# Kernel tuning notes

Hardware: AMD Instinct MI355X
Metric: run time of the kernel (lower is better)

## Reference

```python
import jax, jax.numpy as jnp
import numpy as np

N_Z = 128
N_COMP = 10
N_CLASSES = 10
BS = 8192


def setup_inputs() -> dict:
    key = jax.random.key(0)
    k_z, k_g, k_m = jax.random.split(key, 3)
    z = jax.random.normal(k_z, (BS, N_Z), dtype=jnp.float32)
    y = jax.random.randint(k_g, (BS,), 0, N_CLASSES, dtype=jnp.int64)
    # Gumbel noise replicating torch F.gumbel_softmax internal sampling
    gumbel = jax.random.gumbel(jax.random.fold_in(key, 1), (N_CLASSES, BS, N_COMP), dtype=jnp.float32)
    m = jax.random.normal(k_m, (N_CLASSES, N_COMP, N_Z), dtype=jnp.float32)
    # torch init: L = eye(n_z) per (class, component)
    L = jnp.broadcast_to(jnp.eye(N_Z, dtype=jnp.float32), (N_CLASSES, N_COMP, N_Z, N_Z))
    logits = jnp.zeros((N_CLASSES, N_COMP), dtype=jnp.float32)
    return {"z": z, "y": y, "gumbel": gumbel, "m": m, "L": L, "logits": logits}


def reference(z, y, gumbel, m, L, logits):
    C, K = logits.shape
    # hard gumbel-softmax (tau=1) per class, straight-through
    scores = logits[:, None, :] + gumbel                 # (C, bs, K)
    soft = jax.nn.softmax(scores, axis=-1)               # (C, bs, K)
    hard = jax.nn.one_hot(jnp.argmax(scores, axis=-1), K, dtype=soft.dtype)
    comp_mask = hard + soft - jax.lax.stop_gradient(soft)  # (C, bs, K)
    # every class/component affine: m + z @ L.T -> (C, K, bs, n_z)
    samps = jnp.einsum('bi,ckji->ckbj', z, L) + m[:, :, None, :]
    # select component per (class, sample)
    per_class = jnp.einsum('cbk,ckbj->cbj', comp_mask, samps)  # (C, bs, n_z)
    # select class per sample via one-hot(y)
    y1h = jax.nn.one_hot(y, C, dtype=per_class.dtype)          # (bs, C)
    x = jnp.einsum('bc,cbj->bj', y1h, per_class)               # (bs, n_z)
    return x
```

## Files before the change

### kernel.cpp

```cpp
#include <hip/hip_runtime.h>


#define N_Z 128
#define N_COMP 10
#define N_CLASSES 10
#define N_CK (N_CLASSES * N_COMP)
#define LPITCH 136
#define LIST_CAP 256

typedef __attribute__((ext_vector_type(4))) __bf16 bf16x4;
typedef __attribute__((ext_vector_type(8))) __bf16 bf16x8;
typedef __attribute__((ext_vector_type(4))) float f32x4;

__global__ __launch_bounds__(256) void k_select(
    const int* __restrict__ y, const float* __restrict__ gumbel,
    const float* __restrict__ logits, unsigned char* __restrict__ ck_arr, int bs)
{
    int b = blockIdx.x * 256 + threadIdx.x;
    if (b >= bs) return;
    int c = y[b];
    const float* g  = gumbel + ((size_t)c * bs + b) * N_COMP;
    const float* lg = logits + c * N_COMP;
    float2 g01 = *(const float2*)(g + 0);
    float2 g23 = *(const float2*)(g + 2);
    float2 g45 = *(const float2*)(g + 4);
    float2 g67 = *(const float2*)(g + 6);
    float2 g89 = *(const float2*)(g + 8);
    float sc[N_COMP] = {
        g01.x + lg[0], g01.y + lg[1], g23.x + lg[2], g23.y + lg[3],
        g45.x + lg[4], g45.y + lg[5], g67.x + lg[6], g67.y + lg[7],
        g89.x + lg[8], g89.y + lg[9] };
    float best = sc[0];
    int bi = 0;
    #pragma unroll
    for (int k = 1; k < N_COMP; ++k)
        if (sc[k] > best) { best = sc[k]; bi = k; }
    ck_arr[b] = (unsigned char)(c * N_COMP + bi);
}

__global__ __launch_bounds__(256) void k_mfma(
    const float* __restrict__ z, const float* __restrict__ m,
    const float* __restrict__ L, const unsigned char* __restrict__ ck_arr,
    float* __restrict__ out, int bs)
{
    const int ck = blockIdx.x;
    const int jh = blockIdx.y;

    __shared__ __align__(16) __bf16 Lsb[64 * LPITCH];
    __shared__ int list[LIST_CAP];
    __shared__ int cnt;

    const int t = threadIdx.x;
    if (t == 0) cnt = 0;

    uint4 ckw[2];
    {
        const uint4* ck4 = (const uint4*)ck_arr;
        ckw[0] = ck4[t];
        ckw[1] = ck4[256 + t];
    }
    float4 lv[8];
    {
        const float4* Lg4 = (const float4*)(L + ((size_t)ck * N_Z + jh * 64) * N_Z);
        #pragma unroll
        for (int p = 0; p < 8; ++p) lv[p] = Lg4[p * 256 + t];
    }
    __syncthreads();

    #pragma unroll
    for (int h = 0; h < 2; ++h) {
        int b0 = (h * 256 + t) * 16;
        unsigned w[4] = {ckw[h].x, ckw[h].y, ckw[h].z, ckw[h].w};
        #pragma unroll
        for (int q = 0; q < 4; ++q) {
            #pragma unroll
            for (int e = 0; e < 4; ++e) {
                if (((w[q] >> (8 * e)) & 0xFFu) == (unsigned)ck) {
                    int p2 = atomicAdd(&cnt, 1);
                    if (p2 < LIST_CAP) list[p2] = b0 + q * 4 + e;
                }
            }
        }
    }
    #pragma unroll
    for (int p = 0; p < 8; ++p) {
        int f   = p * 256 + t;
        int row = f >> 5;
        int c4  = f & 31;
        bf16x4 b4 = { (__bf16)lv[p].x, (__bf16)lv[p].y, (__bf16)lv[p].z, (__bf16)lv[p].w };
        *(bf16x4*)&Lsb[row * LPITCH + c4 * 4] = b4;
    }
    __syncthreads();

    const int n = min(cnt, LIST_CAP);
    const int ntiles = (n + 15) >> 4;

    const int wv   = t >> 6;
    const int lane = t & 63;
    const int mn   = lane & 15;
    const int quad = lane >> 4;

    for (int nt = wv; nt < ntiles; nt += 4) {
        const int nb = nt * 16;
        const int sidx = nb + mn;
        const int samp = list[sidx < n ? sidx : n - 1];
        const float* zrow = z + (size_t)samp * N_Z;

        bf16x8 bf[4];
        #pragma unroll
        for (int ks = 0; ks < 4; ++ks) {
            float4 z0 = *(const float4*)(zrow + ks * 32 + quad * 8);
            float4 z1 = *(const float4*)(zrow + ks * 32 + quad * 8 + 4);
            bf16x8 b8 = { (__bf16)z0.x, (__bf16)z0.y, (__bf16)z0.z, (__bf16)z0.w,
                          (__bf16)z1.x, (__bf16)z1.y, (__bf16)z1.z, (__bf16)z1.w };
            bf[ks] = b8;
        }

        #pragma unroll
        for (int mt = 0; mt < 4; ++mt) {
            f32x4 acc = {0.f, 0.f, 0.f, 0.f};
            #pragma unroll
            for (int ks = 0; ks < 4; ++ks) {
                bf16x8 af = *(const bf16x8*)&Lsb[(mt * 16 + mn) * LPITCH + ks * 32 + quad * 8];
                acc = __builtin_amdgcn_mfma_f32_16x16x32_bf16(af, bf[ks], acc, 0, 0, 0);
            }
            if (sidx < n) {
                int j0 = jh * 64 + mt * 16 + quad * 4;
                float4 mv = *(const float4*)(m + ck * N_Z + j0);
                float4 o;
                o.x = acc.x + mv.x;
                o.y = acc.y + mv.y;
                o.z = acc.z + mv.z;
                o.w = acc.w + mv.w;
                *(float4*)(out + (size_t)list[sidx] * N_Z + j0) = o;
            }
        }
    }
}

extern "C" void kernel_launch(void* const* d_in, const int* in_sizes, int n_in,
                              void* d_out, int out_size, void* d_ws, size_t ws_size,
                              hipStream_t stream)
{
    const float* z      = (const float*)d_in[0];
    const int*   y      = (const int*)d_in[1];
    const float* gumbel = (const float*)d_in[2];
    const float* m      = (const float*)d_in[3];
    const float* L      = (const float*)d_in[4];
    const float* logits = (const float*)d_in[5];
    float* out = (float*)d_out;

    const int bs = in_sizes[0] / N_Z;

    unsigned char* ck_arr = (unsigned char*)d_ws;

    k_select<<<(bs + 255) / 256, 256, 0, stream>>>(y, gumbel, logits, ck_arr, bs);
    k_mfma<<<dim3(N_CK, 2), 256, 0, stream>>>(z, m, L, ck_arr, out, bs);
}
```

Before: 80.64 us.

## Fuse select and MFMA kernels with a device-wide flag barrier, split batch

```diff
diff --git a/kernel.cpp b/kernel.cpp
--- a/kernel.cpp
+++ b/kernel.cpp
@@ -7,70 +7,78 @@
 #define N_CK (N_CLASSES * N_COMP)
 #define LPITCH 136
 #define LIST_CAP 256
+#define POISON 0xAAAAAAAAu
 
 typedef __attribute__((ext_vector_type(4))) __bf16 bf16x4;
 typedef __attribute__((ext_vector_type(8))) __bf16 bf16x8;
 typedef __attribute__((ext_vector_type(4))) float f32x4;
 
-__global__ __launch_bounds__(256) void k_select(
-    const int* __restrict__ y, const float* __restrict__ gumbel,
-    const float* __restrict__ logits, unsigned char* __restrict__ ck_arr, int bs)
-{
-    int b = blockIdx.x * 256 + threadIdx.x;
-    if (b >= bs) return;
-    int c = y[b];
-    const float* g  = gumbel + ((size_t)c * bs + b) * N_COMP;
-    const float* lg = logits + c * N_COMP;
-    float2 g01 = *(const float2*)(g + 0);
-    float2 g23 = *(const float2*)(g + 2);
-    float2 g45 = *(const float2*)(g + 4);
-    float2 g67 = *(const float2*)(g + 6);
-    float2 g89 = *(const float2*)(g + 8);
-    float sc[N_COMP] = {
-        g01.x + lg[0], g01.y + lg[1], g23.x + lg[2], g23.y + lg[3],
-        g45.x + lg[4], g45.y + lg[5], g67.x + lg[6], g67.y + lg[7],
-        g89.x + lg[8], g89.y + lg[9] };
-    float best = sc[0];
-    int bi = 0;
-    #pragma unroll
-    for (int k = 1; k < N_COMP; ++k)
-        if (sc[k] > best) { best = sc[k]; bi = k; }
-    ck_arr[b] = (unsigned char)(c * N_COMP + bi);
-}
-
-__global__ __launch_bounds__(256) void k_mfma(
-    const float* __restrict__ z, const float* __restrict__ m,
-    const float* __restrict__ L, const unsigned char* __restrict__ ck_arr,
-    float* __restrict__ out, int bs)
+__global__ __launch_bounds__(256, 2) void k_fused(
+    const float* __restrict__ z, const int* __restrict__ y,
+    const float* __restrict__ gumbel, const float* __restrict__ m,
+    const float* __restrict__ L, const float* __restrict__ logits,
+    float* __restrict__ out, unsigned* __restrict__ flag,
+    unsigned char* __restrict__ ck_arr, int bs)
 {
     const int ck = blockIdx.x;
     const int jh = blockIdx.y;
+    const int bh = blockIdx.z;
+    const int t  = threadIdx.x;
+    const int pid = ck + N_CK * (jh + 2 * bh);
 
     __shared__ __align__(16) __bf16 Lsb[64 * LPITCH];
     __shared__ int list[LIST_CAP];
     __shared__ int cnt;
 
-    const int t = threadIdx.x;
     if (t == 0) cnt = 0;
 
-    uint4 ckw[2];
-    {
-        const uint4* ck4 = (const uint4*)ck_arr;
-        ckw[0] = ck4[t];
-        ckw[1] = ck4[256 + t];
-    }
     float4 lv[8];
     {
         const float4* Lg4 = (const float4*)(L + ((size_t)ck * N_Z + jh * 64) * N_Z);
         #pragma unroll
         for (int p = 0; p < 8; ++p) lv[p] = Lg4[p * 256 + t];
     }
+
+    const unsigned nprod = (unsigned)(bs >> 8);
+    if ((unsigned)pid < nprod) {
+        int b = pid * 256 + t;
+        int c = y[b];
+        const float* g  = gumbel + ((size_t)c * bs + b) * N_COMP;
+        const float* lg = logits + c * N_COMP;
+        float2 g01 = *(const float2*)(g + 0);
+        float2 g23 = *(const float2*)(g + 2);
+        float2 g45 = *(const float2*)(g + 4);
+        float2 g67 = *(const float2*)(g + 6);
+        float2 g89 = *(const float2*)(g + 8);
+        float sc[N_COMP] = {
+            g01.x + lg[0], g01.y + lg[1], g23.x + lg[2], g23.y + lg[3],
+            g45.x + lg[4], g45.y + lg[5], g67.x + lg[6], g67.y + lg[7],
+            g89.x + lg[8], g89.y + lg[9] };
+        float best = sc[0];
+        int bi = 0;
+        #pragma unroll
+        for (int k = 1; k < N_COMP; ++k)
+            if (sc[k] > best) { best = sc[k]; bi = k; }
+        ck_arr[b] = (unsigned char)(c * N_COMP + bi);
+        __threadfence();
+        __syncthreads();
+        if (t == 0)
+            __hip_atomic_fetch_add(flag, 1u, __ATOMIC_RELEASE, __HIP_MEMORY_SCOPE_AGENT);
+    }
+
+    if (t == 0) {
+        long it = 0;
+        while ((__hip_atomic_load(flag, __ATOMIC_ACQUIRE, __HIP_MEMORY_SCOPE_AGENT)
+                - POISON) < nprod && ++it < (1L << 26)) {}
+    }
     __syncthreads();
 
-    #pragma unroll
-    for (int h = 0; h < 2; ++h) {
-        int b0 = (h * 256 + t) * 16;
-        unsigned w[4] = {ckw[h].x, ckw[h].y, ckw[h].z, ckw[h].w};
+    {
+        const int half = bs >> 1;
+        const uint4* ck4 = (const uint4*)(ck_arr + bh * half);
+        uint4 v = ck4[t];
+        int b0 = bh * half + t * 16;
+        unsigned w[4] = {v.x, v.y, v.z, v.w};
         #pragma unroll
         for (int q = 0; q < 4; ++q) {
             #pragma unroll
@@ -132,7 +140,7 @@
                 o.y = acc.y + mv.y;
                 o.z = acc.z + mv.z;
                 o.w = acc.w + mv.w;
-                *(float4*)(out + (size_t)list[sidx] * N_Z + j0) = o;
+                *(float4*)(out + (size_t)samp * N_Z + j0) = o;
             }
         }
     }
@@ -152,8 +160,9 @@
 
     const int bs = in_sizes[0] / N_Z;
 
-    unsigned char* ck_arr = (unsigned char*)d_ws;
+    unsigned*      flag   = (unsigned*)d_ws;
+    unsigned char* ck_arr = (unsigned char*)d_ws + 64;
 
-    k_select<<<(bs + 255) / 256, 256, 0, stream>>>(y, gumbel, logits, ck_arr, bs);
-    k_mfma<<<dim3(N_CK, 2), 256, 0, stream>>>(z, m, L, ck_arr, out, bs);
+    k_fused<<<dim3(N_CK, 2, 2), 256, 0, stream>>>(
+        z, y, gumbel, m, L, logits, out, flag, ck_arr, bs);
 }
```

After: 109.7 us. 1.36x slower.

## Fuse component selection into MFMA kernel and split batch into slices

Applied to the files above, without the earlier changes.

```diff
diff --git a/kernel.cpp b/kernel.cpp
--- a/kernel.cpp
+++ b/kernel.cpp
@@ -5,6 +5,7 @@
 #define N_COMP 10
 #define N_CLASSES 10
 #define N_CK (N_CLASSES * N_COMP)
+#define NSL 4
 #define LPITCH 136
 #define LIST_CAP 256
 
@@ -12,76 +13,71 @@
 typedef __attribute__((ext_vector_type(8))) __bf16 bf16x8;
 typedef __attribute__((ext_vector_type(4))) float f32x4;
 
-__global__ __launch_bounds__(256) void k_select(
-    const int* __restrict__ y, const float* __restrict__ gumbel,
-    const float* __restrict__ logits, unsigned char* __restrict__ ck_arr, int bs)
-{
-    int b = blockIdx.x * 256 + threadIdx.x;
-    if (b >= bs) return;
-    int c = y[b];
-    const float* g  = gumbel + ((size_t)c * bs + b) * N_COMP;
-    const float* lg = logits + c * N_COMP;
-    float2 g01 = *(const float2*)(g + 0);
-    float2 g23 = *(const float2*)(g + 2);
-    float2 g45 = *(const float2*)(g + 4);
-    float2 g67 = *(const float2*)(g + 6);
-    float2 g89 = *(const float2*)(g + 8);
-    float sc[N_COMP] = {
-        g01.x + lg[0], g01.y + lg[1], g23.x + lg[2], g23.y + lg[3],
-        g45.x + lg[4], g45.y + lg[5], g67.x + lg[6], g67.y + lg[7],
-        g89.x + lg[8], g89.y + lg[9] };
-    float best = sc[0];
-    int bi = 0;
-    #pragma unroll
-    for (int k = 1; k < N_COMP; ++k)
-        if (sc[k] > best) { best = sc[k]; bi = k; }
-    ck_arr[b] = (unsigned char)(c * N_COMP + bi);
-}
-
-__global__ __launch_bounds__(256) void k_mfma(
-    const float* __restrict__ z, const float* __restrict__ m,
-    const float* __restrict__ L, const unsigned char* __restrict__ ck_arr,
+__global__ __launch_bounds__(256, 2) void k_all(
+    const float* __restrict__ z, const int* __restrict__ y,
+    const float* __restrict__ gumbel, const float* __restrict__ m,
+    const float* __restrict__ L, const float* __restrict__ logits,
     float* __restrict__ out, int bs)
 {
-    const int ck = blockIdx.x;
-    const int jh = blockIdx.y;
+    const int ck  = blockIdx.x;
+    const int jh  = blockIdx.y;
+    const int slc = blockIdx.z;
+    const int c   = ck / N_COMP;
+    const int kk  = ck - c * N_COMP;
+    const int t   = threadIdx.x;
 
     __shared__ __align__(16) __bf16 Lsb[64 * LPITCH];
     __shared__ int list[LIST_CAP];
     __shared__ int cnt;
 
-    const int t = threadIdx.x;
     if (t == 0) cnt = 0;
+    __syncthreads();
 
-    uint4 ckw[2];
-    {
-        const uint4* ck4 = (const uint4*)ck_arr;
-        ckw[0] = ck4[t];
-        ckw[1] = ck4[256 + t];
-    }
     float4 lv[8];
     {
         const float4* Lg4 = (const float4*)(L + ((size_t)ck * N_Z + jh * 64) * N_Z);
         #pragma unroll
         for (int p = 0; p < 8; ++p) lv[p] = Lg4[p * 256 + t];
     }
-    __syncthreads();
 
+    float lg[N_COMP];
     #pragma unroll
-    for (int h = 0; h < 2; ++h) {
-        int b0 = (h * 256 + t) * 16;
-        unsigned w[4] = {ckw[h].x, ckw[h].y, ckw[h].z, ckw[h].w};
+    for (int k = 0; k < N_COMP; ++k) lg[k] = logits[c * N_COMP + k];
+
+    {
+        const int ssz   = bs / NSL;
+        const int sbase = slc * ssz;
+        const uint4* y4 = (const uint4*)(y + sbase);
+        uint4 ya = y4[2 * t], yb = y4[2 * t + 1];
+        int ys[8] = {(int)ya.x, (int)ya.y, (int)ya.z, (int)ya.w,
+                     (int)yb.x, (int)yb.y, (int)yb.z, (int)yb.w};
         #pragma unroll
-        for (int q = 0; q < 4; ++q) {
-            #pragma unroll
-            for (int e = 0; e < 4; ++e) {
-                if (((w[q] >> (8 * e)) & 0xFFu) == (unsigned)ck) {
+        for (int e = 0; e < 8; ++e) {
+            if (ys[e] == c) {
+                int s = sbase + t * 8 + e;
+                const float* g = gumbel + ((size_t)c * bs + s) * N_COMP;
+                float2 g01 = *(const float2*)(g + 0);
+                float2 g23 = *(const float2*)(g + 2);
+                float2 g45 = *(const float2*)(g + 4);
+                float2 g67 = *(const float2*)(g + 6);
+                float2 g89 = *(const float2*)(g + 8);
+                float sc[N_COMP] = {
+                    g01.x + lg[0], g01.y + lg[1], g23.x + lg[2], g23.y + lg[3],
+                    g45.x + lg[4], g45.y + lg[5], g67.x + lg[6], g67.y + lg[7],
+                    g89.x + lg[8], g89.y + lg[9] };
+                float best = sc[0];
+                int bi = 0;
+                #pragma unroll
+                for (int k = 1; k < N_COMP; ++k)
+                    if (sc[k] > best) { best = sc[k]; bi = k; }
+                if (bi == kk) {
                     int p2 = atomicAdd(&cnt, 1);
-                    if (p2 < LIST_CAP) list[p2] = b0 + q * 4 + e;
+                    if (p2 < LIST_CAP) list[p2] = s;
                 }
             }
         }
     }
+
     #pragma unroll
     for (int p = 0; p < 8; ++p) {
         int f   = p * 256 + t;
@@ -132,7 +128,7 @@
                 o.y = acc.y + mv.y;
                 o.z = acc.z + mv.z;
                 o.w = acc.w + mv.w;
-                *(float4*)(out + (size_t)list[sidx] * N_Z + j0) = o;
+                *(float4*)(out + (size_t)samp * N_Z + j0) = o;
             }
         }
     }
@@ -152,8 +148,6 @@
 
     const int bs = in_sizes[0] / N_Z;
 
-    unsigned char* ck_arr = (unsigned char*)d_ws;
-
-    k_select<<<(bs + 255) / 256, 256, 0, stream>>>(y, gumbel, logits, ck_arr, bs);
-    k_mfma<<<dim3(N_CK, 2), 256, 0, stream>>>(z, m, L, ck_arr, out, bs);
+    k_all<<<dim3(N_CK, 2, NSL), 256, 0, stream>>>(
+        z, y, gumbel, m, L, logits, out, bs);
 }
```

Result: no change. 80.16 us, median of 2 (-0.6%).
